# Kernel tuning notes

Measured on AMD Instinct MI355X. Metric: run time of the kernel, lower is better.

## Reference

```python
import jax, jax.numpy as jnp
import numpy as np

B, F, L = 256, 32, 4096  # batch, num_filters, length == input_dim


def setup_inputs() -> dict:
    key = jax.random.key(0)
    k1, k2, k3 = jax.random.split(key, 3)
    x = jax.random.normal(k1, (B, L), dtype=jnp.float32)
    window_params = jax.random.normal(k2, (F, L), dtype=jnp.float32) * 0.02
    # original init: linspace(0.1, 0.5, F).unsqueeze(0); use same deterministic init
    freq_params = jnp.linspace(0.1, 0.5, F, dtype=jnp.float32)[None, :]
    return {"x": x, "window_params": window_params, "freq_params": freq_params}


def reference(x, window_params, freq_params):
    # x: [B, L]; window_params: [F, L]; freq_params: [1, F]
    length = x.shape[-1]
    windows = jax.nn.softmax(window_params, axis=-1)            # [F, L]
    freqs = jax.nn.sigmoid(freq_params)[0] * 0.5                # [F]
    n = jnp.arange(length, dtype=jnp.float32)                   # [L]
    # complex modulation atoms for ALL filters at once (single batched FFT)
    phase = -2.0 * jnp.pi * freqs[:, None] * n[None, :]         # [F, L]
    modulation = jnp.exp(1j * phase.astype(jnp.complex64))      # [F, L] complex64
    atoms = windows.astype(jnp.complex64) * modulation          # [F, L]
    Xf = jnp.fft.fft(x, axis=-1)                                # [B, L]
    Af = jnp.fft.fft(atoms, axis=-1)                            # [F, L]
    # circular correlation of x with each atom, all filters batched
    prod = Xf[:, None, :] * jnp.conj(Af)[None, :, :]            # [B, F, L]
    return jnp.real(jnp.fft.ifft(prod, axis=-1)).astype(x.dtype)  # [B, F, L]
```

## Files before the change

### kernel.cpp

```cpp
#include <hip/hip_runtime.h>
#include <math.h>

#define B 256
#define F 32
#define L 4096
#define NT 256
#define TWO_PI 6.28318530717958647692f

__device__ __forceinline__ int pidx(int i) { return i + (i >> 4); }

__device__ __forceinline__ int rev3(int i) {
    return ((i & 15) << 8) | (i & 0xF0) | (i >> 8);
}

__device__ __forceinline__ float2 cmul(float2 a, float2 b) {
    return make_float2(a.x * b.x - a.y * b.y, a.x * b.y + a.y * b.x);
}
__device__ __forceinline__ float2 cmulc(float2 a, float cr, float ci) {
    return make_float2(a.x * cr - a.y * ci, a.x * ci + a.y * cr);
}

template<int SGN>
__device__ __forceinline__ void dft4(float2& a, float2& b, float2& c, float2& d) {
    const float s = (float)SGN;
    float2 t0 = make_float2(a.x + c.x, a.y + c.y);
    float2 t1 = make_float2(a.x - c.x, a.y - c.y);
    float2 t2 = make_float2(b.x + d.x, b.y + d.y);
    float2 t3 = make_float2(b.x - d.x, b.y - d.y);
    float2 it3 = make_float2(-s * t3.y, s * t3.x);
    a = make_float2(t0.x + t2.x, t0.y + t2.y);
    c = make_float2(t0.x - t2.x, t0.y - t2.y);
    b = make_float2(t1.x + it3.x, t1.y + it3.y);
    d = make_float2(t1.x - it3.x, t1.y - it3.y);
}

template<int SGN>
__device__ __forceinline__ void dft16(float2 v[16]) {
    const float s = (float)SGN;
    const float C1 = 0.92387953251128675613f;
    const float S1 = 0.38268343236508977173f;
    const float C2 = 0.70710678118654752440f;
    #pragma unroll
    for (int c = 0; c < 4; ++c) dft4<SGN>(v[c], v[c + 4], v[c + 8], v[c + 12]);
    v[5]  = cmulc(v[5],  C1,  s * S1);
    v[6]  = cmulc(v[6],  C2,  s * C2);
    v[7]  = cmulc(v[7],  S1,  s * C1);
    v[9]  = cmulc(v[9],  C2,  s * C2);
    v[10] = make_float2(-s * v[10].y, s * v[10].x);
    v[11] = cmulc(v[11], -C2, s * C2);
    v[13] = cmulc(v[13], S1,  s * C1);
    v[14] = cmulc(v[14], -C2, s * C2);
    v[15] = cmulc(v[15], -C1, -s * S1);
    float2 o[16];
    #pragma unroll
    for (int m = 0; m < 4; ++m) {
        float2 a = v[4*m], b = v[4*m+1], c = v[4*m+2], d = v[4*m+3];
        dft4<SGN>(a, b, c, d);
        o[m] = a; o[m+4] = b; o[m+8] = c; o[m+12] = d;
    }
    #pragma unroll
    for (int i = 0; i < 16; ++i) v[i] = o[i];
}

__device__ __forceinline__ void twiddle_pow(float2 v[16], float2 w1) {
    float2 w = w1;
    #pragma unroll
    for (int q = 1; q < 16; ++q) {
        v[q] = cmul(v[q], w);
        w = cmul(w, w1);
    }
}

__device__ __forceinline__ void build_twid(float2* twp, float sgn, int tid) {
    float ang = sgn * (TWO_PI / (float)L) * (float)tid;
    float sv, cv;
    sincosf(ang, &sv, &cv);
    twp[pidx(tid)] = make_float2(cv, sv);
}

__global__ void __launch_bounds__(NT) atoms_kernel(const float* __restrict__ wp,
                                                   const float* __restrict__ fp,
                                                   float2* __restrict__ Cs) {
    __shared__ float2 lds[L + (L >> 4)];
    __shared__ float2 twp[272];
    __shared__ float2 bufa[L];
    __shared__ float2 bufb[L];
    __shared__ float red[4];
    const int j = blockIdx.x;
    const int t = threadIdx.x;
    build_twid(twp, -1.0f, t);

    for (int half = 0; half < 2; ++half) {
        const int f = 2 * j + half;
        const float* row = wp + (size_t)f * L;
        float m = -INFINITY;
        for (int i = t; i < L; i += NT) m = fmaxf(m, row[i]);
        #pragma unroll
        for (int off = 32; off; off >>= 1) m = fmaxf(m, __shfl_down(m, off));
        if ((t & 63) == 0) red[t >> 6] = m;
        __syncthreads();
        m = fmaxf(fmaxf(red[0], red[1]), fmaxf(red[2], red[3]));
        __syncthreads();
        float sum = 0.0f;
        for (int i = t; i < L; i += NT) sum += expf(row[i] - m);
        #pragma unroll
        for (int off = 32; off; off >>= 1) sum += __shfl_down(sum, off);
        if ((t & 63) == 0) red[t >> 6] = sum;
        __syncthreads();
        sum = red[0] + red[1] + red[2] + red[3];
        __syncthreads();
        const float inv = 1.0f / sum;
        const float fr = 0.5f / (1.0f + expf(-fp[f]));
        const float w0 = -TWO_PI * fr;
        #pragma unroll
        for (int c = 0; c < 16; ++c) {
            int n = t + 256 * c;
            float e = expf(row[n] - m) * inv;
            float sv, cv;
            sincosf(w0 * (float)n, &sv, &cv);
            lds[pidx(n)] = make_float2(e * cv, e * sv);
        }
        __syncthreads();
        float2 v[16];
        #pragma unroll
        for (int q = 0; q < 16; ++q) v[q] = lds[pidx(t + 256 * q)];
        dft16<-1>(v);
        twiddle_pow(v, twp[pidx(t)]);
        #pragma unroll
        for (int p = 0; p < 16; ++p) lds[pidx(t + 256 * p)] = v[p];
        __syncthreads();
        {
            const int base = (t >> 4) * 256 + (t & 15);
            #pragma unroll
            for (int q = 0; q < 16; ++q) v[q] = lds[pidx(base + 16 * q)];
            dft16<-1>(v);
            twiddle_pow(v, twp[pidx(16 * (t & 15))]);
            #pragma unroll
            for (int p = 0; p < 16; ++p) lds[pidx(base + 16 * p)] = v[p];
        }
        __syncthreads();
        #pragma unroll
        for (int q = 0; q < 16; ++q) v[q] = lds[pidx(16 * t + q)];
        dft16<-1>(v);
        float2* buf = half ? bufb : bufa;
        #pragma unroll
        for (int r = 0; r < 16; ++r) buf[rev3(16 * t + r)] = v[r];
        __syncthreads();
    }
    const float sc = 0.5f / (float)L;
    float2* co = Cs + (size_t)j * L;
    #pragma unroll
    for (int c = 0; c < 16; ++c) {
        int i = t + 256 * c;
        int k = rev3(i);
        int km = (L - k) & (L - 1);
        float2 a0k = bufa[k], a0m = bufa[km];
        float2 a1k = bufb[k], a1m = bufb[km];
        float g0r = a0k.x + a0m.x, g0i = a0m.y - a0k.y;
        float g1r = a1k.x + a1m.x, g1i = a1m.y - a1k.y;
        co[i] = make_float2((g0r - g1i) * sc, (g0i + g1r) * sc);
    }
}

__global__ void __launch_bounds__(NT) fftx_kernel(const float* __restrict__ x,
                                                  float2* __restrict__ Xs) {
    __shared__ float2 lds[L + (L >> 4)];
    __shared__ float2 twp[272];
    const int bb = blockIdx.x;
    const int t = threadIdx.x;
    build_twid(twp, -1.0f, t);
    const float* row = x + (size_t)bb * L;
    float2 v[16];
    #pragma unroll
    for (int q = 0; q < 16; ++q) v[q] = make_float2(row[t + 256 * q], 0.0f);
    dft16<-1>(v);
    twiddle_pow(v, twp[pidx(t)]);
    #pragma unroll
    for (int p = 0; p < 16; ++p) lds[pidx(t + 256 * p)] = v[p];
    __syncthreads();
    {
        const int base = (t >> 4) * 256 + (t & 15);
        #pragma unroll
        for (int q = 0; q < 16; ++q) v[q] = lds[pidx(base + 16 * q)];
        dft16<-1>(v);
        twiddle_pow(v, twp[pidx(16 * (t & 15))]);
        #pragma unroll
        for (int p = 0; p < 16; ++p) lds[pidx(base + 16 * p)] = v[p];
    }
    __syncthreads();
    #pragma unroll
    for (int q = 0; q < 16; ++q) v[q] = lds[pidx(16 * t + q)];
    dft16<-1>(v);
    float4* o4 = (float4*)(Xs + (size_t)bb * L + 16 * t);
    #pragma unroll
    for (int h = 0; h < 8; ++h)
        o4[h] = make_float4(v[2*h].x, v[2*h].y, v[2*h+1].x, v[2*h+1].y);
}

__global__ void __launch_bounds__(NT) corr_kernel(const float2* __restrict__ Xs,
                                                  const float2* __restrict__ Cs,
                                                  float* __restrict__ out) {
    __shared__ float2 lds[L + (L >> 4)];
    __shared__ float2 twp[272];
    const int blk = blockIdx.x;
    const int b = blk >> 4;
    const int jf = blk & 15;
    const int t = threadIdx.x;
    build_twid(twp, 1.0f, t);

    const float2* xr = Xs + (size_t)b * L;
    const float2* cr = Cs + (size_t)jf * L;

    float2 v[16];
    const float4* x4 = (const float4*)(xr + 16 * t);
    const float4* c4 = (const float4*)(cr + 16 * t);
    #pragma unroll
    for (int h = 0; h < 8; ++h) {
        float4 xa = x4[h];
        float4 ca = c4[h];
        v[2*h]   = cmul(make_float2(xa.x, xa.y), make_float2(ca.x, ca.y));
        v[2*h+1] = cmul(make_float2(xa.z, xa.w), make_float2(ca.z, ca.w));
    }
    dft16<1>(v);
    #pragma unroll
    for (int r = 0; r < 16; ++r) lds[pidx(16 * t + r)] = v[r];
    __syncthreads();
    {
        const int base = (t >> 4) * 256 + (t & 15);
        #pragma unroll
        for (int q = 0; q < 16; ++q) v[q] = lds[pidx(base + 16 * q)];
        twiddle_pow(v, twp[pidx(16 * (t & 15))]);
        dft16<1>(v);
        #pragma unroll
        for (int r = 0; r < 16; ++r) lds[pidx(base + 16 * r)] = v[r];
    }
    __syncthreads();
    {
        #pragma unroll
        for (int q = 0; q < 16; ++q) v[q] = lds[pidx(t + 256 * q)];
        twiddle_pow(v, twp[pidx(t)]);
        dft16<1>(v);
        float* o0 = out + ((size_t)b * F + 2 * jf) * L;
        float* o1 = o0 + L;
        #pragma unroll
        for (int r = 0; r < 16; ++r) {
            __builtin_nontemporal_store(v[r].x, o0 + t + 256 * r);
            __builtin_nontemporal_store(v[r].y, o1 + t + 256 * r);
        }
    }
}

extern "C" void kernel_launch(void* const* d_in, const int* in_sizes, int n_in,
                              void* d_out, int out_size, void* d_ws, size_t ws_size,
                              hipStream_t stream) {
    (void)in_sizes; (void)n_in; (void)out_size; (void)ws_size;
    const float* x  = (const float*)d_in[0];
    const float* wp = (const float*)d_in[1];
    const float* fp = (const float*)d_in[2];
    float* out = (float*)d_out;

    float2* Xs = (float2*)d_ws;
    float2* Cs = Xs + (size_t)B * L;

    atoms_kernel<<<dim3(F / 2), dim3(NT), 0, stream>>>(wp, fp, Cs);
    fftx_kernel<<<dim3(B), dim3(NT), 0, stream>>>(x, Xs);
    corr_kernel<<<dim3(B * F / 2), dim3(NT), 0, stream>>>(Xs, Cs, out);
}
```

Baseline: 203.3 us.

## Merge atom and input FFTs into one launch and use precomputed middle-stage twiddles

The atom FFTs and the x-row FFTs now run in a single prep kernel with one block per filter plus one per batch row. Before, 16 blocks each handled two filters serially. A small pair kernel then combines the two real-packed atom spectra from global memory. The middle FFT stage reads per-thread twiddles from a shared-memory table instead of computing them by repeated complex multiplication. The cost is an extra workspace buffer and a global round trip for the atom spectra. The main cost it targets is the serial, low-parallelism atoms kernel sitting on the critical path.

Result: faster. 186.3 us (-8.4%).

```diff
diff --git a/kernel.cpp b/kernel.cpp
--- a/kernel.cpp
+++ b/kernel.cpp
@@ -71,130 +71,126 @@
     }
 }
 
-__device__ __forceinline__ void build_twid(float2* twp, float sgn, int tid) {
-    float ang = sgn * (TWO_PI / (float)L) * (float)tid;
+template<int SGN>
+__device__ __forceinline__ void build_tables(float2* twp, float2* T1, int t) {
     float sv, cv;
-    sincosf(ang, &sv, &cv);
-    twp[pidx(tid)] = make_float2(cv, sv);
-}
-
-__global__ void __launch_bounds__(NT) atoms_kernel(const float* __restrict__ wp,
-                                                   const float* __restrict__ fp,
-                                                   float2* __restrict__ Cs) {
+    float a1 = (float)SGN * (TWO_PI / (float)L) * (float)t;
+    sincosf(a1, &sv, &cv);
+    twp[pidx(t)] = make_float2(cv, sv);
+    float a2 = (float)SGN * (TWO_PI / 256.0f) * (float)((t >> 4) * (t & 15));
+    sincosf(a2, &sv, &cv);
+    T1[17 * (t >> 4) + (t & 15)] = make_float2(cv, sv);
+}
+
+__device__ __forceinline__ void fft_dif_fwd(float2 v[16], float2* lds,
+                                            const float2* twp, const float2* T1, int t) {
+    dft16<-1>(v);
+    twiddle_pow(v, twp[pidx(t)]);
+    #pragma unroll
+    for (int p = 0; p < 16; ++p) lds[pidx(t + 256 * p)] = v[p];
+    __syncthreads();
+    const int base = (t >> 4) * 256 + (t & 15);
+    #pragma unroll
+    for (int q = 0; q < 16; ++q) v[q] = lds[pidx(base + 16 * q)];
+    dft16<-1>(v);
+    {
+        const float2* Tr = T1 + 17 * (t & 15);
+        #pragma unroll
+        for (int p = 1; p < 16; ++p) v[p] = cmul(v[p], Tr[p]);
+    }
+    #pragma unroll
+    for (int p = 0; p < 16; ++p) lds[pidx(base + 16 * p)] = v[p];
+    __syncthreads();
+    #pragma unroll
+    for (int q = 0; q < 16; ++q) v[q] = lds[pidx(16 * t + q)];
+    dft16<-1>(v);
+}
+
+__global__ void __launch_bounds__(NT) prep_kernel(const float* __restrict__ x,
+                                                  const float* __restrict__ wp,
+                                                  const float* __restrict__ fp,
+                                                  float2* __restrict__ Xs,
+                                                  float2* __restrict__ Anat) {
     __shared__ float2 lds[L + (L >> 4)];
     __shared__ float2 twp[272];
-    __shared__ float2 bufa[L];
-    __shared__ float2 bufb[L];
+    __shared__ float2 T1[272];
     __shared__ float red[4];
+    const int t = threadIdx.x;
+    build_tables<-1>(twp, T1, t);
+    float2 v[16];
+
+    if (blockIdx.x < F) {
+        const int f = blockIdx.x;
+        const float* row = wp + (size_t)f * L;
+        float rv[16];
+        #pragma unroll
+        for (int c = 0; c < 16; ++c) rv[c] = row[t + 256 * c];
+        float m = -INFINITY;
+        #pragma unroll
+        for (int c = 0; c < 16; ++c) m = fmaxf(m, rv[c]);
+        #pragma unroll
+        for (int off = 32; off; off >>= 1) m = fmaxf(m, __shfl_down(m, off));
+        if ((t & 63) == 0) red[t >> 6] = m;
+        __syncthreads();
+        m = fmaxf(fmaxf(red[0], red[1]), fmaxf(red[2], red[3]));
+        __syncthreads();
+        float s = 0.0f;
+        #pragma unroll
+        for (int c = 0; c < 16; ++c) { rv[c] = expf(rv[c] - m); s += rv[c]; }
+        #pragma unroll
+        for (int off = 32; off; off >>= 1) s += __shfl_down(s, off);
+        if ((t & 63) == 0) red[t >> 6] = s;
+        __syncthreads();
+        s = red[0] + red[1] + red[2] + red[3];
+        const float inv = 1.0f / s;
+        const float fr = 0.5f / (1.0f + expf(-fp[f]));
+        const float w0 = -TWO_PI * fr;
+        #pragma unroll
+        for (int c = 0; c < 16; ++c) {
+            const int n = t + 256 * c;
+            const float e = rv[c] * inv;
+            float sv, cv;
+            sincosf(w0 * (float)n, &sv, &cv);
+            v[c] = make_float2(e * cv, e * sv);
+        }
+        __syncthreads();
+        fft_dif_fwd(v, lds, twp, T1, t);
+        float2* an = Anat + (size_t)f * L;
+        #pragma unroll
+        for (int r = 0; r < 16; ++r) an[rev3(16 * t + r)] = v[r];
+    } else {
+        const int bb = blockIdx.x - F;
+        const float* row = x + (size_t)bb * L;
+        #pragma unroll
+        for (int q = 0; q < 16; ++q) v[q] = make_float2(row[t + 256 * q], 0.0f);
+        __syncthreads();
+        fft_dif_fwd(v, lds, twp, T1, t);
+        float4* o4 = (float4*)(Xs + (size_t)bb * L + 16 * t);
+        #pragma unroll
+        for (int h = 0; h < 8; ++h)
+            o4[h] = make_float4(v[2*h].x, v[2*h].y, v[2*h+1].x, v[2*h+1].y);
+    }
+}
+
+__global__ void __launch_bounds__(NT) pair_kernel(const float2* __restrict__ Anat,
+                                                  float2* __restrict__ Cs) {
     const int j = blockIdx.x;
     const int t = threadIdx.x;
-    build_twid(twp, -1.0f, t);
-
-    for (int half = 0; half < 2; ++half) {
-        const int f = 2 * j + half;
-        const float* row = wp + (size_t)f * L;
-        float m = -INFINITY;
-        for (int i = t; i < L; i += NT) m = fmaxf(m, row[i]);
-        #pragma unroll
-        for (int off = 32; off; off >>= 1) m = fmaxf(m, __shfl_down(m, off));
-        if ((t & 63) == 0) red[t >> 6] = m;
-        __syncthreads();
-        m = fmaxf(fmaxf(red[0], red[1]), fmaxf(red[2], red[3]));
-        __syncthreads();
-        float sum = 0.0f;
-        for (int i = t; i < L; i += NT) sum += expf(row[i] - m);
-        #pragma unroll
-        for (int off = 32; off; off >>= 1) sum += __shfl_down(sum, off);
-        if ((t & 63) == 0) red[t >> 6] = sum;
-        __syncthreads();
-        sum = red[0] + red[1] + red[2] + red[3];
-        __syncthreads();
-        const float inv = 1.0f / sum;
-        const float fr = 0.5f / (1.0f + expf(-fp[f]));
-        const float w0 = -TWO_PI * fr;
-        #pragma unroll
-        for (int c = 0; c < 16; ++c) {
-            int n = t + 256 * c;
-            float e = expf(row[n] - m) * inv;
-            float sv, cv;
-            sincosf(w0 * (float)n, &sv, &cv);
-            lds[pidx(n)] = make_float2(e * cv, e * sv);
-        }
-        __syncthreads();
-        float2 v[16];
-        #pragma unroll
-        for (int q = 0; q < 16; ++q) v[q] = lds[pidx(t + 256 * q)];
-        dft16<-1>(v);
-        twiddle_pow(v, twp[pidx(t)]);
-        #pragma unroll
-        for (int p = 0; p < 16; ++p) lds[pidx(t + 256 * p)] = v[p];
-        __syncthreads();
-        {
-            const int base = (t >> 4) * 256 + (t & 15);
-            #pragma unroll
-            for (int q = 0; q < 16; ++q) v[q] = lds[pidx(base + 16 * q)];
-            dft16<-1>(v);
-            twiddle_pow(v, twp[pidx(16 * (t & 15))]);
-            #pragma unroll
-            for (int p = 0; p < 16; ++p) lds[pidx(base + 16 * p)] = v[p];
-        }
-        __syncthreads();
-        #pragma unroll
-        for (int q = 0; q < 16; ++q) v[q] = lds[pidx(16 * t + q)];
-        dft16<-1>(v);
-        float2* buf = half ? bufb : bufa;
-        #pragma unroll
-        for (int r = 0; r < 16; ++r) buf[rev3(16 * t + r)] = v[r];
-        __syncthreads();
-    }
+    const float2* a0 = Anat + (size_t)(2 * j) * L;
+    const float2* a1 = a0 + L;
     const float sc = 0.5f / (float)L;
     float2* co = Cs + (size_t)j * L;
     #pragma unroll
     for (int c = 0; c < 16; ++c) {
-        int i = t + 256 * c;
-        int k = rev3(i);
-        int km = (L - k) & (L - 1);
-        float2 a0k = bufa[k], a0m = bufa[km];
-        float2 a1k = bufb[k], a1m = bufb[km];
-        float g0r = a0k.x + a0m.x, g0i = a0m.y - a0k.y;
-        float g1r = a1k.x + a1m.x, g1i = a1m.y - a1k.y;
+        const int i = t + 256 * c;
+        const int k = rev3(i);
+        const int km = (L - k) & (L - 1);
+        const float2 a0k = a0[k], a0m = a0[km];
+        const float2 a1k = a1[k], a1m = a1[km];
+        const float g0r = a0k.x + a0m.x, g0i = a0m.y - a0k.y;
+        const float g1r = a1k.x + a1m.x, g1i = a1m.y - a1k.y;
         co[i] = make_float2((g0r - g1i) * sc, (g0i + g1r) * sc);
     }
-}
-
-__global__ void __launch_bounds__(NT) fftx_kernel(const float* __restrict__ x,
-                                                  float2* __restrict__ Xs) {
-    __shared__ float2 lds[L + (L >> 4)];
-    __shared__ float2 twp[272];
-    const int bb = blockIdx.x;
-    const int t = threadIdx.x;
-    build_twid(twp, -1.0f, t);
-    const float* row = x + (size_t)bb * L;
-    float2 v[16];
-    #pragma unroll
-    for (int q = 0; q < 16; ++q) v[q] = make_float2(row[t + 256 * q], 0.0f);
-    dft16<-1>(v);
-    twiddle_pow(v, twp[pidx(t)]);
-    #pragma unroll
-    for (int p = 0; p < 16; ++p) lds[pidx(t + 256 * p)] = v[p];
-    __syncthreads();
-    {
-        const int base = (t >> 4) * 256 + (t & 15);
-        #pragma unroll
-        for (int q = 0; q < 16; ++q) v[q] = lds[pidx(base + 16 * q)];
-        dft16<-1>(v);
-        twiddle_pow(v, twp[pidx(16 * (t & 15))]);
-        #pragma unroll
-        for (int p = 0; p < 16; ++p) lds[pidx(base + 16 * p)] = v[p];
-    }
-    __syncthreads();
-    #pragma unroll
-    for (int q = 0; q < 16; ++q) v[q] = lds[pidx(16 * t + q)];
-    dft16<-1>(v);
-    float4* o4 = (float4*)(Xs + (size_t)bb * L + 16 * t);
-    #pragma unroll
-    for (int h = 0; h < 8; ++h)
-        o4[h] = make_float4(v[2*h].x, v[2*h].y, v[2*h+1].x, v[2*h+1].y);
 }
 
 __global__ void __launch_bounds__(NT) corr_kernel(const float2* __restrict__ Xs,
@@ -202,11 +198,12 @@
                                                   float* __restrict__ out) {
     __shared__ float2 lds[L + (L >> 4)];
     __shared__ float2 twp[272];
+    __shared__ float2 T1[272];
     const int blk = blockIdx.x;
     const int b = blk >> 4;
     const int jf = blk & 15;
     const int t = threadIdx.x;
-    build_twid(twp, 1.0f, t);
+    build_tables<1>(twp, T1, t);
 
     const float2* xr = Xs + (size_t)b * L;
     const float2* cr = Cs + (size_t)jf * L;
@@ -216,8 +213,8 @@
     const float4* c4 = (const float4*)(cr + 16 * t);
     #pragma unroll
     for (int h = 0; h < 8; ++h) {
-        float4 xa = x4[h];
-        float4 ca = c4[h];
+        const float4 xa = x4[h];
+        const float4 ca = c4[h];
         v[2*h]   = cmul(make_float2(xa.x, xa.y), make_float2(ca.x, ca.y));
         v[2*h+1] = cmul(make_float2(xa.z, xa.w), make_float2(ca.z, ca.w));
     }
@@ -227,9 +224,11 @@
     __syncthreads();
     {
         const int base = (t >> 4) * 256 + (t & 15);
+        const float2* Tr = T1 + 17 * (t & 15);
         #pragma unroll
         for (int q = 0; q < 16; ++q) v[q] = lds[pidx(base + 16 * q)];
-        twiddle_pow(v, twp[pidx(16 * (t & 15))]);
+        #pragma unroll
+        for (int q = 1; q < 16; ++q) v[q] = cmul(v[q], Tr[q]);
         dft16<1>(v);
         #pragma unroll
         for (int r = 0; r < 16; ++r) lds[pidx(base + 16 * r)] = v[r];
@@ -259,10 +258,11 @@
     const float* fp = (const float*)d_in[2];
     float* out = (float*)d_out;
 
-    float2* Xs = (float2*)d_ws;
-    float2* Cs = Xs + (size_t)B * L;
-
-    atoms_kernel<<<dim3(F / 2), dim3(NT), 0, stream>>>(wp, fp, Cs);
-    fftx_kernel<<<dim3(B), dim3(NT), 0, stream>>>(x, Xs);
+    float2* Xs   = (float2*)d_ws;
+    float2* Cs   = Xs + (size_t)B * L;
+    float2* Anat = Cs + (size_t)(F / 2) * L;
+
+    prep_kernel<<<dim3(F + B), dim3(NT), 0, stream>>>(x, wp, fp, Xs, Anat);
+    pair_kernel<<<dim3(F / 2), dim3(NT), 0, stream>>>(Anat, Cs);
     corr_kernel<<<dim3(B * F / 2), dim3(NT), 0, stream>>>(Xs, Cs, out);
 }
```
